# Optimization experiments

Measured on AMD Instinct MI355X. Metric: run time of the kernel, lower is better.

## Reference

```python
import jax, jax.numpy as jnp
import numpy as np

SCORE_THR = 0.005   # score_thres is None in init -> default 0.005
IOU_THR = 0.5
TOPK = 1024         # fixed pre-NMS candidate cap (JAX needs static shapes)


def setup_inputs() -> dict:
    key = jax.random.key(0)
    # (B, 4+nc, N_anchors): 16 images, 80 classes, 33600 anchors (1280x1280, strides 8/16/32)
    x = jax.random.normal(key, (16, 84, 33600), dtype=jnp.float32)
    return {"x": x}


def _pairwise_iou(b):
    # b: (K, 4) xyxy. Same math as torchvision.ops.box_iou.
    lt = jnp.maximum(b[:, None, :2], b[None, :, :2])   # (K, K, 2)
    rb = jnp.minimum(b[:, None, 2:], b[None, :, 2:])   # (K, K, 2)
    wh = jnp.clip(rb - lt, 0.0)
    inter = wh[..., 0] * wh[..., 1]
    area = (b[:, 2] - b[:, 0]) * (b[:, 3] - b[:, 1])
    union = area[:, None] + area[None, :] - inter
    return inter / jnp.maximum(union, 1e-9)


def _nms_single(boxes, svals, cids):
    # boxes (N,4); svals (N,) with -inf where score <= threshold; cids (N,) int
    top_s, idx = jax.lax.top_k(svals, TOPK)            # score-descending candidates
    b = boxes[idx]                                      # (K, 4)
    c = cids[idx]                                       # (K,)
    valid = top_s > SCORE_THR                           # thresholded-out slots are -inf
    iou = _pairwise_iou(b)                              # (K, K)
    ar = jnp.arange(TOPK)

    def body(i, keep):
        # greedy NMS: box i (if still kept) suppresses lower-scored boxes with IoU > thr
        sup = (iou[i] > IOU_THR) & (ar > i) & keep[i]
        return keep & ~sup

    keep = jax.lax.fori_loop(0, TOPK, body, valid)
    out = jnp.concatenate([b, top_s[:, None], c[:, None].astype(jnp.float32)], axis=1)  # (K, 6)
    out = jnp.where(keep[:, None], out, 0.0)            # padded fixed-size result
    return out, keep


def reference(x):
    xt = jnp.transpose(x, (0, 2, 1))                    # (B, N, 4+nc)
    boxes, scores = xt[..., :4], xt[..., 4:]
    svals = scores.max(-1)                              # (B, N)
    cids = scores.argmax(-1)                            # (B, N)
    svals = jnp.where(svals > SCORE_THR, svals, -jnp.inf)  # score-threshold mask
    out, keep = jax.vmap(_nms_single)(boxes, svals, cids)
    # out: (B, TOPK, 6) zero-padded [xyxy, score, cls]; keep: (B, TOPK) validity mask
    return out, keep
```

## Files before the change

kernel.cpp:

```cpp
#include <hip/hip_runtime.h>
#include <cstdint>
#include <cstddef>

#define NB 16
#define NC 84
#define NA 33600
#define NCLS 80
#define TOPK 1024
#define NBIN 8192
#define CANDCAP 8192
#define SELCAP 2048
#define SCORE_THR 0.005f
#define IOU_THR 0.5f

__device__ __forceinline__ unsigned mono_u32(float f) {
    unsigned u = __float_as_uint(f);
    return (u & 0x80000000u) ? ~u : (u | 0x80000000u);
}
__device__ __forceinline__ float key_val(uint64_t k) {
    unsigned u = (unsigned)(k >> 32);
    u = (u & 0x80000000u) ? (u & 0x7FFFFFFFu) : ~u;
    return __uint_as_float(u);
}
__device__ __forceinline__ int key_idx(uint64_t k) {
    return (int)(~(uint32_t)(k & 0xFFFFFFFFu));
}

__global__ __launch_bounds__(256) void score_kernel(const float* __restrict__ x,
                                                    float* __restrict__ sval,
                                                    int* __restrict__ cid) {
    int gid = blockIdx.x * 256 + threadIdx.x;
    if (gid >= NB * (NA / 4)) return;
    int b = gid / (NA / 4);
    int q = gid - b * (NA / 4);
    const float4* p = (const float4*)(x + (size_t)b * NC * NA + (size_t)4 * NA) + q;
    float4 best = p[0];
    int4 bc = {0, 0, 0, 0};
#pragma unroll 4
    for (int c = 1; c < NCLS; ++c) {
        float4 v = p[(size_t)c * (NA / 4)];
        if (v.x > best.x) { best.x = v.x; bc.x = c; }
        if (v.y > best.y) { best.y = v.y; bc.y = c; }
        if (v.z > best.z) { best.z = v.z; bc.z = c; }
        if (v.w > best.w) { best.w = v.w; bc.w = c; }
    }
    float4 s;
    s.x = (best.x > SCORE_THR) ? best.x : -INFINITY;
    s.y = (best.y > SCORE_THR) ? best.y : -INFINITY;
    s.z = (best.z > SCORE_THR) ? best.z : -INFINITY;
    s.w = (best.w > SCORE_THR) ? best.w : -INFINITY;
    ((float4*)sval)[gid] = s;
    ((int4*)cid)[gid] = bc;
}

__global__ __launch_bounds__(256) void hist_kernel(const float* __restrict__ sval,
                                                   unsigned* __restrict__ hist) {
    int b = blockIdx.x >> 4;
    int sub = blockIdx.x & 15;
    int t = threadIdx.x;
    __shared__ unsigned h[NBIN];
    for (int i = t; i < NBIN; i += 256) h[i] = 0;
    __syncthreads();
    int a0 = sub * (NA / 16), a1 = a0 + (NA / 16);
    const float* sv = sval + (size_t)b * NA;
    for (int a = a0 + t; a < a1; a += 256)
        atomicAdd(&h[mono_u32(sv[a]) >> 19], 1u);
    __syncthreads();
    for (int i = t; i < NBIN; i += 256)
        if (h[i]) atomicAdd(&hist[b * NBIN + i], h[i]);
}

__global__ __launch_bounds__(256) void scan_kernel(const unsigned* __restrict__ hist,
                                                   unsigned* __restrict__ cutbin) {
    int b = blockIdx.x;
    int t = threadIdx.x;
    __shared__ unsigned csum[256];
    const unsigned* h = hist + b * NBIN;
    unsigned local = 0;
#pragma unroll 8
    for (int q = 0; q < 32; ++q) local += h[NBIN - 1 - (t * 32 + q)];
    csum[t] = local;
    __syncthreads();
    for (int off = 1; off < 256; off <<= 1) {
        unsigned v = (t >= off) ? csum[t - off] : 0u;
        __syncthreads();
        csum[t] += v;
        __syncthreads();
    }
    unsigned incl = csum[t], excl = incl - local;
    if (excl < TOPK && incl >= TOPK) {
        unsigned cum = excl;
        for (int q = 0; q < 32; ++q) {
            unsigned bin = NBIN - 1 - (t * 32 + q);
            unsigned c = h[bin];
            if (cum + c >= TOPK) { cutbin[b] = bin; break; }
            cum += c;
        }
    }
}

__global__ __launch_bounds__(256) void compact_kernel(const float* __restrict__ sval,
                                                      const unsigned* __restrict__ cutbin,
                                                      uint64_t* __restrict__ cand,
                                                      unsigned* __restrict__ cnt) {
    int gid = blockIdx.x * 256 + threadIdx.x;
    int b = gid / NA;
    int a = gid - b * NA;
    int b_first = (blockIdx.x * 256) / NA;
    int seg = b - b_first;
    __shared__ unsigned lcnt[2], lbase[2];
    __shared__ uint64_t k0[256], k1[256];
    if (threadIdx.x < 2) lcnt[threadIdx.x] = 0;
    __syncthreads();
    unsigned u = mono_u32(sval[gid]);
    if ((u >> 19) >= cutbin[b]) {
        unsigned pos = atomicAdd(&lcnt[seg], 1u);
        uint64_t key = ((uint64_t)u << 32) | (uint32_t)(~(uint32_t)a);
        if (seg) k1[pos] = key; else k0[pos] = key;
    }
    __syncthreads();
    if (threadIdx.x == 0 && lcnt[0]) lbase[0] = atomicAdd(&cnt[b_first * 64], lcnt[0]);
    if (threadIdx.x == 1 && lcnt[1]) lbase[1] = atomicAdd(&cnt[(b_first + 1) * 64], lcnt[1]);
    __syncthreads();
    if (threadIdx.x < lcnt[0]) {
        unsigned p = lbase[0] + threadIdx.x;
        if (p < CANDCAP) cand[((size_t)b_first << 13) + p] = k0[threadIdx.x];
    }
    if (threadIdx.x < lcnt[1]) {
        unsigned p = lbase[1] + threadIdx.x;
        if (p < CANDCAP) cand[((size_t)(b_first + 1) << 13) + p] = k1[threadIdx.x];
    }
}

__device__ __forceinline__ void bitonic_desc(uint64_t* A, int n, int tid) {
    for (int k = 2; k <= n; k <<= 1) {
        for (int j = k >> 1; j > 0; j >>= 1) {
            for (int i = tid; i < n; i += 256) {
                int ixj = i ^ j;
                if (ixj > i) {
                    uint64_t a = A[i], b2 = A[ixj];
                    bool up = ((i & k) == 0);
                    if (up ? (a < b2) : (a > b2)) { A[i] = b2; A[ixj] = a; }
                }
            }
            __syncthreads();
        }
    }
}

__global__ __launch_bounds__(256) void sortk_kernel(const uint64_t* __restrict__ cand,
                                                    const unsigned* __restrict__ cnt,
                                                    const unsigned* __restrict__ cutbin,
                                                    float* __restrict__ topval,
                                                    int* __restrict__ topidx) {
    int b = blockIdx.x;
    int t = threadIdx.x;
    __shared__ uint64_t lk[CANDCAP];
    __shared__ uint64_t lsel[SELCAP];
    __shared__ unsigned sh[256];
    __shared__ unsigned snA, snSel, ssubcut;
    unsigned C = cnt[b * 64];
    if (C > CANDCAP) C = CANDCAP;
    unsigned cb = cutbin[b];

    for (int i = t; i < CANDCAP; i += 256)
        lk[i] = (i < (int)C) ? cand[((size_t)b << 13) + i] : 0ULL;
    for (int i = t; i < SELCAP; i += 256) lsel[i] = 0ULL;
    for (int i = t; i < 256; i += 256) sh[i] = 0;
    if (t == 0) { snA = 0; snSel = 0; }
    __syncthreads();

    unsigned myA = 0;
    for (int i = t; i < (int)C; i += 256) {
        unsigned u = (unsigned)(lk[i] >> 32);
        if ((u >> 19) > cb) myA++;
        else atomicAdd(&sh[(u >> 11) & 255u], 1u);
    }
    atomicAdd(&snA, myA);
    __syncthreads();

    if (t == 0) {
        unsigned r = TOPK - snA;
        unsigned cum = 0, sc = 0;
        for (int s = 255; s >= 0; --s) {
            cum += sh[s];
            if (cum >= r) { sc = (unsigned)s; break; }
        }
        ssubcut = sc;
    }
    __syncthreads();
    unsigned subcut = ssubcut;

    int lane = t & 63;
    for (int i = t; i < CANDCAP; i += 256) {
        unsigned u = (unsigned)(lk[i] >> 32);
        unsigned bin = u >> 19;
        bool sel = (bin > cb) || (bin == cb && ((u >> 11) & 255u) >= subcut);
        uint64_t mask = __ballot(sel);
        if (mask) {
            int ldr = __ffsll((unsigned long long)mask) - 1;
            unsigned base = 0;
            if (lane == ldr) base = atomicAdd(&snSel, (unsigned)__popcll(mask));
            base = __shfl(base, ldr, 64);
            if (sel) {
                unsigned p = base + (unsigned)__popcll(mask & ((1ULL << lane) - 1ULL));
                if (p < SELCAP) lsel[p] = lk[i];
            }
        }
    }
    __syncthreads();
    unsigned nSel = snSel;

    uint64_t* buf;
    if (nSel <= SELCAP) { bitonic_desc(lsel, SELCAP, t); buf = lsel; }
    else                { bitonic_desc(lk, CANDCAP, t);  buf = lk;  }

    for (int i = t; i < TOPK; i += 256) {
        uint64_t key = buf[i];
        topval[b * TOPK + i] = key_val(key);
        topidx[b * TOPK + i] = key_idx(key);
    }
}

__global__ __launch_bounds__(256) void boxes_kernel(const float* __restrict__ x,
                                                    const int* __restrict__ cid,
                                                    const int* __restrict__ tidx,
                                                    float* __restrict__ bx1, float* __restrict__ by1,
                                                    float* __restrict__ bx2, float* __restrict__ by2,
                                                    float* __restrict__ bar, int* __restrict__ tcid) {
    int b = blockIdx.x;
    int base = b << 10;
    const float* xb = x + (size_t)b * NC * NA;
    for (int k = threadIdx.x; k < TOPK; k += 256) {
        int idx = tidx[base + k];
        float x1 = xb[idx], y1 = xb[NA + idx], x2 = xb[2 * NA + idx], y2 = xb[3 * NA + idx];
        bx1[base + k] = x1; by1[base + k] = y1;
        bx2[base + k] = x2; by2[base + k] = y2;
        bar[base + k] = (x2 - x1) * (y2 - y1);
        tcid[base + k] = cid[b * NA + idx];
    }
}

#define LDSPAD(j) ((j) + ((j) >> 6))
__global__ __launch_bounds__(256) void maskbuild_kernel(const float* __restrict__ bx1,
                                                        const float* __restrict__ by1,
                                                        const float* __restrict__ bx2,
                                                        const float* __restrict__ by2,
                                                        const float* __restrict__ bar,
                                                        const float* __restrict__ tval,
                                                        uint64_t* __restrict__ M,
                                                        int* __restrict__ rowflag) {
    int b = blockIdx.x >> 6;
    int r0 = (blockIdx.x & 63) << 4;
    int t = threadIdx.x;
    int r = r0 + (t >> 4);
    int w = t & 15;
    int base = b << 10;
    __shared__ float sx1[TOPK + 16], sy1[TOPK + 16], sx2[TOPK + 16], sy2[TOPK + 16], sar[TOPK + 16];
    __shared__ int anyf[256];

    for (int j = t; j < TOPK; j += 256) {
        int ji = LDSPAD(j);
        sx1[ji] = bx1[base + j]; sy1[ji] = by1[base + j];
        sx2[ji] = bx2[base + j]; sy2[ji] = by2[base + j];
        sar[ji] = bar[base + j];
    }
    __syncthreads();

    int ri = LDSPAD(r);
    float ix1 = sx1[ri], iy1 = sy1[ri], ix2 = sx2[ri], iy2 = sy2[ri], ia = sar[ri];
    uint64_t m = 0;
#pragma unroll 8
    for (int jj = 0; jj < 64; ++jj) {
        int j = (w << 6) + jj;
        int ji = w * 65 + jj;
        float ltx = fmaxf(ix1, sx1[ji]);
        float lty = fmaxf(iy1, sy1[ji]);
        float rbx = fminf(ix2, sx2[ji]);
        float rby = fminf(iy2, sy2[ji]);
        float ww = fmaxf(rbx - ltx, 0.0f);
        float hh = fmaxf(rby - lty, 0.0f);
        float inter = ww * hh;
        float uni = ia + sar[ji] - inter;
        float iou = inter / fmaxf(uni, 1e-9f);
        if (j > r && iou > IOU_THR) m |= (1ULL << jj);
    }
    M[((size_t)(base + r) << 4) + w] = m;
    anyf[t] = (m != 0ULL);
    __syncthreads();
    if (w == 0) {
        int any = 0;
#pragma unroll
        for (int q = 0; q < 16; ++q) any |= anyf[t + q];
        bool valid = tval[base + r] > SCORE_THR;
        rowflag[base + r] = (any && valid) ? 1 : 0;
    }
}

__global__ __launch_bounds__(64) void sweep_kernel(const uint64_t* __restrict__ M,
                                                   const int* __restrict__ rowflag,
                                                   const float* __restrict__ tval,
                                                   const int* __restrict__ tcid,
                                                   const float* __restrict__ bx1,
                                                   const float* __restrict__ by1,
                                                   const float* __restrict__ bx2,
                                                   const float* __restrict__ by2,
                                                   float* __restrict__ out) {
    int b = blockIdx.x;
    int l = threadIdx.x;
    int base = b << 10;
    int w = l & 15, g = l >> 4;
    __shared__ int list[TOPK];

    float tv[16];
#pragma unroll
    for (int s = 0; s < 16; ++s) tv[s] = tval[base + (s << 6) + l];

    uint64_t vword = 0;
#pragma unroll
    for (int s = 0; s < 16; ++s) {
        uint64_t bal = __ballot(tv[s] > SCORE_THR);
        if (l == s) vword = bal;
    }

    int cnt = 0;
#pragma unroll
    for (int s = 0; s < 16; ++s) {
        int flag = rowflag[base + (s << 6) + l];
        uint64_t m = __ballot(flag != 0);
        if (flag) {
            int pos = cnt + __popcll(m & ((1ULL << l) - 1ULL));
            list[pos] = (s << 6) + l;
        }
        cnt += __popcll(m);
    }
    __syncthreads();

    uint64_t remv = 0;
    for (int chunk = 0; chunk < cnt; chunk += 64) {
        int m = min(64, cnt - chunk);
        int idx_l = chunk + l;
        int myi = list[(idx_l < cnt) ? idx_l : 0];
        uint64_t rows[16];
#pragma unroll
        for (int q = 0; q < 16; ++q) {
            int it = chunk + q * 4 + g;
            int it2 = (it < cnt) ? it : 0;
            uint64_t v = M[((size_t)(base + list[it2]) << 4) + w];
            rows[q] = (it < cnt) ? v : 0ULL;
        }
        for (int r = 0; r < m; ++r) {
            int i = __shfl(myi, r, 64);
            uint64_t row = __shfl(rows[r >> 2], ((r & 3) << 4) + w, 64);
            uint64_t rb = __shfl(remv, i >> 6, 64);
            bool kept = !((rb >> (i & 63)) & 1ULL);
            remv |= (kept && l < 16) ? row : 0ULL;
        }
    }

    uint64_t kf = vword & ~remv;
#pragma unroll
    for (int s = 0; s < 16; ++s) {
        uint64_t kw = __shfl(kf, s, 64);
        bool kp = (kw >> l) & 1ULL;
        int k = (s << 6) + l;
        float x1 = bx1[base + k], y1 = by1[base + k];
        float x2 = bx2[base + k], y2 = by2[base + k];
        float* po = out + ((size_t)(base + k)) * 6;
        po[0] = kp ? x1 : 0.0f;
        po[1] = kp ? y1 : 0.0f;
        po[2] = kp ? x2 : 0.0f;
        po[3] = kp ? y2 : 0.0f;
        po[4] = kp ? tv[s] : 0.0f;
        po[5] = kp ? (float)tcid[base + k] : 0.0f;
        out[(size_t)NB * TOPK * 6 + base + k] = kp ? 1.0f : 0.0f;
    }
}

extern "C" void kernel_launch(void* const* d_in, const int* in_sizes, int n_in,
                              void* d_out, int out_size, void* d_ws, size_t ws_size,
                              hipStream_t stream) {
    const float* x = (const float*)d_in[0];
    float* out = (float*)d_out;
    char* ws = (char*)d_ws;

    size_t off = 0;
    auto alloc = [&](size_t bytes) { void* p = ws + off; off = (off + bytes + 255) & ~(size_t)255; return p; };
    float*    sval    = (float*)alloc((size_t)NB * NA * 4);
    int*      cid     = (int*)alloc((size_t)NB * NA * 4);
    unsigned* hist    = (unsigned*)alloc((size_t)NB * NBIN * 4);
    unsigned* cutbin  = (unsigned*)alloc(NB * 4);
    unsigned* cnt     = (unsigned*)alloc((size_t)NB * 64 * 4);
    uint64_t* cand    = (uint64_t*)alloc((size_t)NB * CANDCAP * 8);
    float*    tval    = (float*)alloc((size_t)NB * TOPK * 4);
    int*      tidx    = (int*)alloc((size_t)NB * TOPK * 4);
    float*    bx1     = (float*)alloc((size_t)NB * TOPK * 4);
    float*    by1     = (float*)alloc((size_t)NB * TOPK * 4);
    float*    bx2     = (float*)alloc((size_t)NB * TOPK * 4);
    float*    by2     = (float*)alloc((size_t)NB * TOPK * 4);
    float*    bar     = (float*)alloc((size_t)NB * TOPK * 4);
    int*      tcid    = (int*)alloc((size_t)NB * TOPK * 4);
    int*      rowflag = (int*)alloc((size_t)NB * TOPK * 4);
    uint64_t* M       = (uint64_t*)alloc((size_t)NB * TOPK * 16 * 8);

    hipMemsetAsync(hist, 0, (size_t)NB * NBIN * 4, stream);
    hipMemsetAsync(cnt, 0, (size_t)NB * 64 * 4, stream);

    score_kernel<<<NB * (NA / 4) / 256, 256, 0, stream>>>(x, sval, cid);
    hist_kernel<<<NB * 16, 256, 0, stream>>>(sval, hist);
    scan_kernel<<<NB, 256, 0, stream>>>(hist, cutbin);
    compact_kernel<<<NB * NA / 256, 256, 0, stream>>>(sval, cutbin, cand, cnt);
    sortk_kernel<<<NB, 256, 0, stream>>>(cand, cnt, cutbin, tval, tidx);
    boxes_kernel<<<NB, 256, 0, stream>>>(x, cid, tidx, bx1, by1, bx2, by2, bar, tcid);
    maskbuild_kernel<<<NB * 64, 256, 0, stream>>>(bx1, by1, bx2, by2, bar, tval, M, rowflag);
    sweep_kernel<<<NB, 64, 0, stream>>>(M, rowflag, tval, tcid, bx1, by1, bx2, by2, out);
}
```

Measured before the change: 412.0 us.

## Fuse score+histogram and scan+compact+sort+gather kernels; skip lower-triangle IoU tiles

The score/argmax kernel now also builds the per-image shared-memory histogram, so the separate histogram pass over sval goes away. The scan, candidate compaction, top-k sort and box gather are merged into one per-image kernel. That kernel compacts with wave-ballot atomics into LDS instead of going through a global candidate buffer. The mask-build kernel remaps threads and skips IoU work for 64-column blocks that lie entirely at or below the current row. Together this removes four launches plus intermediate global traffic, but compaction now runs on only 16 blocks.

```diff
diff --git a/kernel.cpp b/kernel.cpp
--- a/kernel.cpp
+++ b/kernel.cpp
@@ -12,6 +12,7 @@
 #define SELCAP 2048
 #define SCORE_THR 0.005f
 #define IOU_THR 0.5f
+#define SBLK 33
 
 __device__ __forceinline__ unsigned mono_u32(float f) {
     unsigned u = __float_as_uint(f);
@@ -26,110 +27,46 @@
     return (int)(~(uint32_t)(k & 0xFFFFFFFFu));
 }
 
-__global__ __launch_bounds__(256) void score_kernel(const float* __restrict__ x,
-                                                    float* __restrict__ sval,
-                                                    int* __restrict__ cid) {
-    int gid = blockIdx.x * 256 + threadIdx.x;
-    if (gid >= NB * (NA / 4)) return;
-    int b = gid / (NA / 4);
-    int q = gid - b * (NA / 4);
-    const float4* p = (const float4*)(x + (size_t)b * NC * NA + (size_t)4 * NA) + q;
-    float4 best = p[0];
-    int4 bc = {0, 0, 0, 0};
-#pragma unroll 4
-    for (int c = 1; c < NCLS; ++c) {
-        float4 v = p[(size_t)c * (NA / 4)];
-        if (v.x > best.x) { best.x = v.x; bc.x = c; }
-        if (v.y > best.y) { best.y = v.y; bc.y = c; }
-        if (v.z > best.z) { best.z = v.z; bc.z = c; }
-        if (v.w > best.w) { best.w = v.w; bc.w = c; }
-    }
-    float4 s;
-    s.x = (best.x > SCORE_THR) ? best.x : -INFINITY;
-    s.y = (best.y > SCORE_THR) ? best.y : -INFINITY;
-    s.z = (best.z > SCORE_THR) ? best.z : -INFINITY;
-    s.w = (best.w > SCORE_THR) ? best.w : -INFINITY;
-    ((float4*)sval)[gid] = s;
-    ((int4*)cid)[gid] = bc;
-}
-
-__global__ __launch_bounds__(256) void hist_kernel(const float* __restrict__ sval,
-                                                   unsigned* __restrict__ hist) {
-    int b = blockIdx.x >> 4;
-    int sub = blockIdx.x & 15;
+__global__ __launch_bounds__(256) void score_hist_kernel(const float* __restrict__ x,
+                                                         float* __restrict__ sval,
+                                                         int* __restrict__ cid,
+                                                         unsigned* __restrict__ hist) {
+    int b = blockIdx.x / SBLK;
+    int blk = blockIdx.x - b * SBLK;
     int t = threadIdx.x;
     __shared__ unsigned h[NBIN];
     for (int i = t; i < NBIN; i += 256) h[i] = 0;
     __syncthreads();
-    int a0 = sub * (NA / 16), a1 = a0 + (NA / 16);
-    const float* sv = sval + (size_t)b * NA;
-    for (int a = a0 + t; a < a1; a += 256)
-        atomicAdd(&h[mono_u32(sv[a]) >> 19], 1u);
-    __syncthreads();
+
+    int q = blk * 256 + t;
+    if (q < NA / 4) {
+        const float4* p = (const float4*)(x + (size_t)b * NC * NA + (size_t)4 * NA) + q;
+        float4 best = p[0];
+        int4 bc = {0, 0, 0, 0};
+#pragma unroll 4
+        for (int c = 1; c < NCLS; ++c) {
+            float4 v = p[(size_t)c * (NA / 4)];
+            if (v.x > best.x) { best.x = v.x; bc.x = c; }
+            if (v.y > best.y) { best.y = v.y; bc.y = c; }
+            if (v.z > best.z) { best.z = v.z; bc.z = c; }
+            if (v.w > best.w) { best.w = v.w; bc.w = c; }
+        }
+        float4 s;
+        s.x = (best.x > SCORE_THR) ? best.x : -INFINITY;
+        s.y = (best.y > SCORE_THR) ? best.y : -INFINITY;
+        s.z = (best.z > SCORE_THR) ? best.z : -INFINITY;
+        s.w = (best.w > SCORE_THR) ? best.w : -INFINITY;
+        ((float4*)(sval + (size_t)b * NA))[q] = s;
+        ((int4*)(cid + (size_t)b * NA))[q] = bc;
+        atomicAdd(&h[mono_u32(s.x) >> 19], 1u);
+        atomicAdd(&h[mono_u32(s.y) >> 19], 1u);
+        atomicAdd(&h[mono_u32(s.z) >> 19], 1u);
+        atomicAdd(&h[mono_u32(s.w) >> 19], 1u);
+    }
+    __syncthreads();
+    unsigned* gh = hist + (size_t)b * NBIN;
     for (int i = t; i < NBIN; i += 256)
-        if (h[i]) atomicAdd(&hist[b * NBIN + i], h[i]);
-}
-
-__global__ __launch_bounds__(256) void scan_kernel(const unsigned* __restrict__ hist,
-                                                   unsigned* __restrict__ cutbin) {
-    int b = blockIdx.x;
-    int t = threadIdx.x;
-    __shared__ unsigned csum[256];
-    const unsigned* h = hist + b * NBIN;
-    unsigned local = 0;
-#pragma unroll 8
-    for (int q = 0; q < 32; ++q) local += h[NBIN - 1 - (t * 32 + q)];
-    csum[t] = local;
-    __syncthreads();
-    for (int off = 1; off < 256; off <<= 1) {
-        unsigned v = (t >= off) ? csum[t - off] : 0u;
-        __syncthreads();
-        csum[t] += v;
-        __syncthreads();
-    }
-    unsigned incl = csum[t], excl = incl - local;
-    if (excl < TOPK && incl >= TOPK) {
-        unsigned cum = excl;
-        for (int q = 0; q < 32; ++q) {
-            unsigned bin = NBIN - 1 - (t * 32 + q);
-            unsigned c = h[bin];
-            if (cum + c >= TOPK) { cutbin[b] = bin; break; }
-            cum += c;
-        }
-    }
-}
-
-__global__ __launch_bounds__(256) void compact_kernel(const float* __restrict__ sval,
-                                                      const unsigned* __restrict__ cutbin,
-                                                      uint64_t* __restrict__ cand,
-                                                      unsigned* __restrict__ cnt) {
-    int gid = blockIdx.x * 256 + threadIdx.x;
-    int b = gid / NA;
-    int a = gid - b * NA;
-    int b_first = (blockIdx.x * 256) / NA;
-    int seg = b - b_first;
-    __shared__ unsigned lcnt[2], lbase[2];
-    __shared__ uint64_t k0[256], k1[256];
-    if (threadIdx.x < 2) lcnt[threadIdx.x] = 0;
-    __syncthreads();
-    unsigned u = mono_u32(sval[gid]);
-    if ((u >> 19) >= cutbin[b]) {
-        unsigned pos = atomicAdd(&lcnt[seg], 1u);
-        uint64_t key = ((uint64_t)u << 32) | (uint32_t)(~(uint32_t)a);
-        if (seg) k1[pos] = key; else k0[pos] = key;
-    }
-    __syncthreads();
-    if (threadIdx.x == 0 && lcnt[0]) lbase[0] = atomicAdd(&cnt[b_first * 64], lcnt[0]);
-    if (threadIdx.x == 1 && lcnt[1]) lbase[1] = atomicAdd(&cnt[(b_first + 1) * 64], lcnt[1]);
-    __syncthreads();
-    if (threadIdx.x < lcnt[0]) {
-        unsigned p = lbase[0] + threadIdx.x;
-        if (p < CANDCAP) cand[((size_t)b_first << 13) + p] = k0[threadIdx.x];
-    }
-    if (threadIdx.x < lcnt[1]) {
-        unsigned p = lbase[1] + threadIdx.x;
-        if (p < CANDCAP) cand[((size_t)(b_first + 1) << 13) + p] = k1[threadIdx.x];
-    }
+        if (h[i]) atomicAdd(&gh[i], h[i]);
 }
 
 __device__ __forceinline__ void bitonic_desc(uint64_t* A, int n, int tid) {
@@ -148,26 +85,71 @@
     }
 }
 
-__global__ __launch_bounds__(256) void sortk_kernel(const uint64_t* __restrict__ cand,
-                                                    const unsigned* __restrict__ cnt,
-                                                    const unsigned* __restrict__ cutbin,
-                                                    float* __restrict__ topval,
-                                                    int* __restrict__ topidx) {
+__global__ __launch_bounds__(256) void select_sort_kernel(const float* __restrict__ sval,
+                                                          const unsigned* __restrict__ hist,
+                                                          const float* __restrict__ x,
+                                                          const int* __restrict__ cid,
+                                                          float* __restrict__ tval,
+                                                          float* __restrict__ bx1, float* __restrict__ by1,
+                                                          float* __restrict__ bx2, float* __restrict__ by2,
+                                                          float* __restrict__ bar, int* __restrict__ tcid) {
     int b = blockIdx.x;
     int t = threadIdx.x;
     __shared__ uint64_t lk[CANDCAP];
     __shared__ uint64_t lsel[SELCAP];
     __shared__ unsigned sh[256];
-    __shared__ unsigned snA, snSel, ssubcut;
-    unsigned C = cnt[b * 64];
-    if (C > CANDCAP) C = CANDCAP;
-    unsigned cb = cutbin[b];
-
-    for (int i = t; i < CANDCAP; i += 256)
-        lk[i] = (i < (int)C) ? cand[((size_t)b << 13) + i] : 0ULL;
+    __shared__ unsigned csum[256];
+    __shared__ unsigned scut, snC, snA, snSel, ssubcut;
+
+    const unsigned* hh = hist + (size_t)b * NBIN;
+    unsigned local = 0;
+#pragma unroll 8
+    for (int q = 0; q < 32; ++q) local += hh[NBIN - 1 - (t * 32 + q)];
+    csum[t] = local;
+    if (t == 0) { snC = 0; snA = 0; snSel = 0; }
+    __syncthreads();
+    for (int off = 1; off < 256; off <<= 1) {
+        unsigned v = (t >= off) ? csum[t - off] : 0u;
+        __syncthreads();
+        csum[t] += v;
+        __syncthreads();
+    }
+    unsigned incl = csum[t], excl = incl - local;
+    if (excl < TOPK && incl >= TOPK) {
+        unsigned cum = excl;
+        for (int q = 0; q < 32; ++q) {
+            unsigned bin = NBIN - 1 - (t * 32 + q);
+            unsigned c = hh[bin];
+            if (cum + c >= TOPK) { scut = bin; break; }
+            cum += c;
+        }
+    }
+    __syncthreads();
+    unsigned cb = scut;
+
+    const float* sv = sval + (size_t)b * NA;
+    int lane = t & 63;
+    for (int i = t; i < NA; i += 256) {
+        unsigned u = mono_u32(sv[i]);
+        bool sel2 = (u >> 19) >= cb;
+        uint64_t mask = __ballot(sel2);
+        if (mask) {
+            int ldr = __ffsll((unsigned long long)mask) - 1;
+            unsigned base = 0;
+            if (lane == ldr) base = atomicAdd(&snC, (unsigned)__popcll(mask));
+            base = __shfl(base, ldr, 64);
+            if (sel2) {
+                unsigned p = base + (unsigned)__popcll(mask & ((1ULL << lane) - 1ULL));
+                if (p < CANDCAP) lk[p] = ((uint64_t)u << 32) | (uint32_t)(~(uint32_t)i);
+            }
+        }
+    }
+    __syncthreads();
+    unsigned C = snC; if (C > CANDCAP) C = CANDCAP;
+
+    for (int i = t; i < CANDCAP; i += 256) if (i >= (int)C) lk[i] = 0ULL;
     for (int i = t; i < SELCAP; i += 256) lsel[i] = 0ULL;
-    for (int i = t; i < 256; i += 256) sh[i] = 0;
-    if (t == 0) { snA = 0; snSel = 0; }
+    sh[t] = 0;
     __syncthreads();
 
     unsigned myA = 0;
@@ -191,18 +173,16 @@
     __syncthreads();
     unsigned subcut = ssubcut;
 
-    int lane = t & 63;
-    for (int i = t; i < CANDCAP; i += 256) {
+    for (int i = t; i < (int)C; i += 256) {
         unsigned u = (unsigned)(lk[i] >> 32);
-        unsigned bin = u >> 19;
-        bool sel = (bin > cb) || (bin == cb && ((u >> 11) & 255u) >= subcut);
-        uint64_t mask = __ballot(sel);
+        bool sel2 = ((u >> 19) > cb) || (((u >> 11) & 255u) >= subcut);
+        uint64_t mask = __ballot(sel2);
         if (mask) {
             int ldr = __ffsll((unsigned long long)mask) - 1;
             unsigned base = 0;
             if (lane == ldr) base = atomicAdd(&snSel, (unsigned)__popcll(mask));
             base = __shfl(base, ldr, 64);
-            if (sel) {
+            if (sel2) {
                 unsigned p = base + (unsigned)__popcll(mask & ((1ULL << lane) - 1ULL));
                 if (p < SELCAP) lsel[p] = lk[i];
             }
@@ -215,29 +195,19 @@
     if (nSel <= SELCAP) { bitonic_desc(lsel, SELCAP, t); buf = lsel; }
     else                { bitonic_desc(lk, CANDCAP, t);  buf = lk;  }
 
+    const float* xb = x + (size_t)b * NC * NA;
+    const int* cidb = cid + (size_t)b * NA;
+    int base_o = b << 10;
     for (int i = t; i < TOPK; i += 256) {
         uint64_t key = buf[i];
-        topval[b * TOPK + i] = key_val(key);
-        topidx[b * TOPK + i] = key_idx(key);
-    }
-}
-
-__global__ __launch_bounds__(256) void boxes_kernel(const float* __restrict__ x,
-                                                    const int* __restrict__ cid,
-                                                    const int* __restrict__ tidx,
-                                                    float* __restrict__ bx1, float* __restrict__ by1,
-                                                    float* __restrict__ bx2, float* __restrict__ by2,
-                                                    float* __restrict__ bar, int* __restrict__ tcid) {
-    int b = blockIdx.x;
-    int base = b << 10;
-    const float* xb = x + (size_t)b * NC * NA;
-    for (int k = threadIdx.x; k < TOPK; k += 256) {
-        int idx = tidx[base + k];
-        float x1 = xb[idx], y1 = xb[NA + idx], x2 = xb[2 * NA + idx], y2 = xb[3 * NA + idx];
-        bx1[base + k] = x1; by1[base + k] = y1;
-        bx2[base + k] = x2; by2[base + k] = y2;
-        bar[base + k] = (x2 - x1) * (y2 - y1);
-        tcid[base + k] = cid[b * NA + idx];
+        tval[base_o + i] = key_val(key);
+        int idx = key_idx(key);
+        float X1 = xb[idx], Y1 = xb[NA + idx];
+        float X2 = xb[2 * NA + idx], Y2 = xb[3 * NA + idx];
+        bx1[base_o + i] = X1; by1[base_o + i] = Y1;
+        bx2[base_o + i] = X2; by2[base_o + i] = Y2;
+        bar[base_o + i] = (X2 - X1) * (Y2 - Y1);
+        tcid[base_o + i] = cidb[idx];
     }
 }
 
@@ -253,8 +223,8 @@
     int b = blockIdx.x >> 6;
     int r0 = (blockIdx.x & 63) << 4;
     int t = threadIdx.x;
-    int r = r0 + (t >> 4);
-    int w = t & 15;
+    int r = r0 + (t & 15);
+    int w = t >> 4;
     int base = b << 10;
     __shared__ float sx1[TOPK + 16], sy1[TOPK + 16], sx2[TOPK + 16], sy2[TOPK + 16], sar[TOPK + 16];
     __shared__ int anyf[256];
@@ -270,30 +240,32 @@
     int ri = LDSPAD(r);
     float ix1 = sx1[ri], iy1 = sy1[ri], ix2 = sx2[ri], iy2 = sy2[ri], ia = sar[ri];
     uint64_t m = 0;
+    if (((w << 6) + 63) > r) {
 #pragma unroll 8
-    for (int jj = 0; jj < 64; ++jj) {
-        int j = (w << 6) + jj;
-        int ji = w * 65 + jj;
-        float ltx = fmaxf(ix1, sx1[ji]);
-        float lty = fmaxf(iy1, sy1[ji]);
-        float rbx = fminf(ix2, sx2[ji]);
-        float rby = fminf(iy2, sy2[ji]);
-        float ww = fmaxf(rbx - ltx, 0.0f);
-        float hh = fmaxf(rby - lty, 0.0f);
-        float inter = ww * hh;
-        float uni = ia + sar[ji] - inter;
-        float iou = inter / fmaxf(uni, 1e-9f);
-        if (j > r && iou > IOU_THR) m |= (1ULL << jj);
+        for (int jj = 0; jj < 64; ++jj) {
+            int j = (w << 6) + jj;
+            int ji = w * 65 + jj;
+            float ltx = fmaxf(ix1, sx1[ji]);
+            float lty = fmaxf(iy1, sy1[ji]);
+            float rbx = fminf(ix2, sx2[ji]);
+            float rby = fminf(iy2, sy2[ji]);
+            float ww = fmaxf(rbx - ltx, 0.0f);
+            float hh = fmaxf(rby - lty, 0.0f);
+            float inter = ww * hh;
+            float uni = ia + sar[ji] - inter;
+            float iou = inter / fmaxf(uni, 1e-9f);
+            if (j > r && iou > IOU_THR) m |= (1ULL << jj);
+        }
     }
     M[((size_t)(base + r) << 4) + w] = m;
     anyf[t] = (m != 0ULL);
     __syncthreads();
-    if (w == 0) {
+    if (t < 16) {
         int any = 0;
 #pragma unroll
-        for (int q = 0; q < 16; ++q) any |= anyf[t + q];
-        bool valid = tval[base + r] > SCORE_THR;
-        rowflag[base + r] = (any && valid) ? 1 : 0;
+        for (int q = 0; q < 16; ++q) any |= anyf[(q << 4) + t];
+        bool valid = tval[base + r0 + t] > SCORE_THR;
+        rowflag[base + r0 + t] = (any && valid) ? 1 : 0;
     }
 }
 
@@ -389,11 +361,7 @@
     float*    sval    = (float*)alloc((size_t)NB * NA * 4);
     int*      cid     = (int*)alloc((size_t)NB * NA * 4);
     unsigned* hist    = (unsigned*)alloc((size_t)NB * NBIN * 4);
-    unsigned* cutbin  = (unsigned*)alloc(NB * 4);
-    unsigned* cnt     = (unsigned*)alloc((size_t)NB * 64 * 4);
-    uint64_t* cand    = (uint64_t*)alloc((size_t)NB * CANDCAP * 8);
     float*    tval    = (float*)alloc((size_t)NB * TOPK * 4);
-    int*      tidx    = (int*)alloc((size_t)NB * TOPK * 4);
     float*    bx1     = (float*)alloc((size_t)NB * TOPK * 4);
     float*    by1     = (float*)alloc((size_t)NB * TOPK * 4);
     float*    bx2     = (float*)alloc((size_t)NB * TOPK * 4);
@@ -404,14 +372,9 @@
     uint64_t* M       = (uint64_t*)alloc((size_t)NB * TOPK * 16 * 8);
 
     hipMemsetAsync(hist, 0, (size_t)NB * NBIN * 4, stream);
-    hipMemsetAsync(cnt, 0, (size_t)NB * 64 * 4, stream);
-
-    score_kernel<<<NB * (NA / 4) / 256, 256, 0, stream>>>(x, sval, cid);
-    hist_kernel<<<NB * 16, 256, 0, stream>>>(sval, hist);
-    scan_kernel<<<NB, 256, 0, stream>>>(hist, cutbin);
-    compact_kernel<<<NB * NA / 256, 256, 0, stream>>>(sval, cutbin, cand, cnt);
-    sortk_kernel<<<NB, 256, 0, stream>>>(cand, cnt, cutbin, tval, tidx);
-    boxes_kernel<<<NB, 256, 0, stream>>>(x, cid, tidx, bx1, by1, bx2, by2, bar, tcid);
+
+    score_hist_kernel<<<NB * SBLK, 256, 0, stream>>>(x, sval, cid, hist);
+    select_sort_kernel<<<NB, 256, 0, stream>>>(sval, hist, x, cid, tval, bx1, by1, bx2, by2, bar, tcid);
     maskbuild_kernel<<<NB * 64, 256, 0, stream>>>(bx1, by1, bx2, by2, bar, tval, M, rowflag);
     sweep_kernel<<<NB, 64, 0, stream>>>(M, rowflag, tval, tcid, bx1, by1, bx2, by2, out);
 }
```

Measured after the change: 442.3 us. 1.07x slower.
